# Performance work log

Hardware: AMD Instinct MI355X
Metric: run time of the kernel (lower is better)

## Reference

```python
import jax, jax.numpy as jnp
import numpy as np

INPUT_SIZE = 256
HIDDEN_SIZE = 256
B, T = 64, 4096


def setup_inputs() -> dict:
    key = jax.random.key(0)
    k_x, k_ih, k_hh, k_b = jax.random.split(key, 4)
    lim = 1.0 / np.sqrt(HIDDEN_SIZE)  # eqx LSTMCell init range
    xs = jax.random.normal(k_x, (B, T, INPUT_SIZE), dtype=jnp.float32)
    W_ih = jax.random.uniform(k_ih, (4 * HIDDEN_SIZE, INPUT_SIZE), minval=-lim, maxval=lim, dtype=jnp.float32)
    W_hh = jax.random.uniform(k_hh, (4 * HIDDEN_SIZE, HIDDEN_SIZE), minval=-lim, maxval=lim, dtype=jnp.float32)
    b = jax.random.uniform(k_b, (4 * HIDDEN_SIZE,), minval=-lim, maxval=lim, dtype=jnp.float32)
    return {"xs": xs, "W_ih": W_ih, "W_hh": W_hh, "b": b}


def reference(xs, W_ih, W_hh, b):
    # xs: [B, T, D]; eqx.nn.LSTMCell math, scanned over time, vectorized over batch.
    Bsz, Tlen, D = xs.shape
    H = W_hh.shape[1]
    # Precompute input contribution for all timesteps in one big GEMM: [T, B, 4H]
    x_gates = jnp.swapaxes(xs @ W_ih.T + b, 0, 1)

    def step(state, xg):
        h, c = state  # each [B, H]
        gates = xg + h @ W_hh.T  # [B, 4H]
        i, f, g, o = jnp.split(gates, 4, axis=-1)
        c = jax.nn.sigmoid(f) * c + jax.nn.sigmoid(i) * jnp.tanh(g)
        h = jax.nn.sigmoid(o) * jnp.tanh(c)
        return (h, c), None

    init = (jnp.zeros((Bsz, H), xs.dtype), jnp.zeros((Bsz, H), xs.dtype))
    (h, c), _ = jax.lax.scan(step, init, x_gates)
    return (h, c)
```

## Files before the change

kernel.cpp:

```cpp
#include <hip/hip_runtime.h>
#include <hip/hip_fp16.h>
#include <stdint.h>


#define LSTM_B 64
#define LSTM_T 4096
#define LSTM_D 256
#define LSTM_H 256

#define WS_HG_OFF (1u << 20)

typedef __attribute__((ext_vector_type(8))) _Float16 half8;
typedef __attribute__((ext_vector_type(4))) float f32x4;
typedef __attribute__((ext_vector_type(4))) uint32_t u32x4;

#define AST64(p, v) __hip_atomic_store((p), (v), __ATOMIC_RELAXED, __HIP_MEMORY_SCOPE_AGENT)
#define BARLG()     asm volatile("s_waitcnt lgkmcnt(0)\n\ts_barrier" ::: "memory")

static __device__ __forceinline__ float sigmoidf_(float x) {
    return 1.0f / (1.0f + __expf(-x));
}
static __device__ __forceinline__ float tanhf_(float x) {
    float ax = fabsf(x);
    float e  = __expf(-2.0f * ax);
    float t  = (1.0f - e) / (1.0f + e);
    return copysignf(t, x);
}

static __device__ __forceinline__ void ld64B_agent(const uint64_t* p, uint64_t* v) {
    u32x4 a, b, c, d;
    asm volatile(
        "global_load_dwordx4 %0, %4, off sc1\n\t"
        "global_load_dwordx4 %1, %4, off offset:16 sc1\n\t"
        "global_load_dwordx4 %2, %4, off offset:32 sc1\n\t"
        "global_load_dwordx4 %3, %4, off offset:48 sc1\n\t"
        "s_waitcnt vmcnt(0)"
        : "=&v"(a), "=&v"(b), "=&v"(c), "=&v"(d)
        : "v"(p) : "memory");
    v[0] = ((uint64_t)a.y << 32) | a.x;
    v[1] = ((uint64_t)a.w << 32) | a.z;
    v[2] = ((uint64_t)b.y << 32) | b.x;
    v[3] = ((uint64_t)b.w << 32) | b.z;
    v[4] = ((uint64_t)c.y << 32) | c.x;
    v[5] = ((uint64_t)c.w << 32) | c.z;
    v[6] = ((uint64_t)d.y << 32) | d.x;
    v[7] = ((uint64_t)d.w << 32) | d.z;
}

__global__ __launch_bounds__(256) void prep_frags(
    const float* __restrict__ W_ih, const float* __restrict__ W_hh,
    uint8_t* __restrict__ ws)
{
    int idx = blockIdx.x * blockDim.x + threadIdx.x;
    uint4* Wp = (uint4*)ws;
    int lane = idx & 63;
    int kk   = (idx >> 6) & 15;
    int T    = idx >> 10;
    int n  = T * 16 + (lane & 15);
    int r  = ((n & 3) << 8) + (n >> 2);
    int kb = 32 * kk + 4 * (lane >> 4);
    uint32_t u[4];
    #pragma unroll
    for (int h = 0; h < 4; ++h) {
        uint32_t lohi[2];
        #pragma unroll
        for (int e = 0; e < 2; ++e) {
            int j = 2 * h + e;
            int k = kb + (j & 3) + 16 * (j >> 2);
            float v = (k < 256) ? W_hh[r * 256 + k] : W_ih[r * 256 + (k - 256)];
            lohi[e] = (uint32_t)__half_as_ushort(__float2half(v));
        }
        u[h] = lohi[0] | (lohi[1] << 16);
    }
    Wp[idx] = make_uint4(u[0], u[1], u[2], u[3]);
    if (idx < 32768) ((uint32_t*)(ws + WS_HG_OFF))[idx] = 0u;
}

__global__ __launch_bounds__(256, 1) void lstm_r15(
    const float* __restrict__ xs,
    const float* __restrict__ bias_g,
    uint8_t* __restrict__ ws,
    float* __restrict__ out)
{
    const int tid = threadIdx.x;
    const int l   = tid & 63;
    const int w   = tid >> 6;
    const int g   = blockIdx.x & 7;
    const int p   = blockIdx.x >> 3;

    const uint4* WF = (const uint4*)ws;
    uint64_t* hg64  = (uint64_t*)(ws + WS_HG_OFF);

    __shared__ uint4 hx[16 * 64];

    uint4 wf[4][16];
    #pragma unroll
    for (int tl = 0; tl < 4; ++tl) {
        int T = p * 16 + w * 4 + tl;
        #pragma unroll
        for (int kk = 0; kk < 16; ++kk)
            wf[tl][kk] = WF[(T * 16 + kk) * 64 + l];
    }
    #pragma unroll
    for (int tl = 0; tl < 4; ++tl)
        #pragma unroll
        for (int kk = 0; kk < 16; ++kk)
            asm volatile("" : "+v"(wf[tl][kk].x), "+v"(wf[tl][kk].y),
                              "+v"(wf[tl][kk].z), "+v"(wf[tl][kk].w));

    const int  c2   = l & 3;
    const int  qa   = l >> 4;
    const bool c2b0 = (c2 & 1) != 0, c2b1 = (c2 & 2) != 0;
    const int  m_ew = 4 * qa + c2;
    float bias[4];
    int   jj[4];
    #pragma unroll
    for (int tl = 0; tl < 4; ++tl) {
        int T    = p * 16 + w * 4 + tl;
        int slot = T * 16 + (l & 15);
        int r    = ((slot & 3) << 8) + (slot >> 2);
        bias[tl] = bias_g[r];
        jj[tl]   = slot >> 2;
    }

    const int m_s = tid >> 4;
    const int d0  = (tid & 15) * 16;
    const float* xrow = xs + (size_t)(8 * g + (m_s & 7)) * LSTM_T * LSTM_D + d0;

    hx[tid]       = make_uint4(0, 0, 0, 0);
    hx[tid + 256] = make_uint4(0, 0, 0, 0);
    hx[tid + 512] = make_uint4(0, 0, 0, 0);
    hx[tid + 768] = make_uint4(0, 0, 0, 0);
    float4 xb[2][4];
    if (m_s < 8) {
        #pragma unroll
        for (int i = 0; i < 4; ++i) {
            float4 xv = ((const float4*)xrow)[i];
            __half2 h0 = __floats2half2_rn(xv.x, xv.y);
            __half2 h1 = __floats2half2_rn(xv.z, xv.w);
            uint64_t v = (uint64_t)__builtin_bit_cast(uint32_t, h0)
                       | ((uint64_t)__builtin_bit_cast(uint32_t, h1) << 32);
            int k0 = 256 + d0 + 4 * i;
            int kk = k0 >> 5, off = k0 & 31;
            int q = (off & 15) >> 2, hi = off >> 4;
            int slot = (m_s + 16 * q) ^ ((2 * kk) & 63);
            *(uint64_t*)((uint8_t*)hx + kk * 1024 + slot * 16 + hi * 8) = v;
        }
        #pragma unroll
        for (int i = 0; i < 4; ++i) xb[0][i] = ((const float4*)(xrow + (size_t)1 * LSTM_D))[i];
        #pragma unroll
        for (int i = 0; i < 4; ++i) xb[1][i] = ((const float4*)(xrow + (size_t)2 * LSTM_D))[i];
    }
    BARLG();

    f32x4 accA[4], accB[4];
    {
        uint4 afx[8];
        #pragma unroll
        for (int kx = 0; kx < 8; ++kx) {
            int kk = kx + 8;
            afx[kx] = hx[kk * 64 + (l ^ ((2 * kk) & 63))];
        }
        #pragma unroll
        for (int tl = 0; tl < 4; ++tl)
            accA[tl] = (f32x4){bias[tl], bias[tl], bias[tl], bias[tl]};
        #pragma unroll
        for (int kx = 0; kx < 8; ++kx) {
            half8 a = __builtin_bit_cast(half8, afx[kx]);
            #pragma unroll
            for (int tl = 0; tl < 4; ++tl)
                accA[tl] = __builtin_amdgcn_mfma_f32_16x16x32_f16(
                    a, __builtin_bit_cast(half8, wf[tl][kx + 8]), accA[tl], 0, 0, 0);
        }
    }

    float cst[4] = {0, 0, 0, 0}, hst[4] = {0, 0, 0, 0};

#define STEP(T_, PAR, ACC_C, ACC_N) do {                                            \
                    \
    uint4 afh[8];                                                                   \
    _Pragma("unroll")                                                               \
    for (int kk = 0; kk < 8; ++kk)                                                  \
        afh[kk] = hx[kk * 64 + (l ^ ((2 * kk) & 63))];                              \
    _Pragma("unroll")                                                               \
    for (int kk = 0; kk < 8; ++kk) {                                                \
        half8 a = __builtin_bit_cast(half8, afh[kk]);                               \
        _Pragma("unroll")                                                           \
        for (int tl = 0; tl < 4; ++tl)                                              \
            ACC_C[tl] = __builtin_amdgcn_mfma_f32_16x16x32_f16(                     \
                a, __builtin_bit_cast(half8, wf[tl][kk]), ACC_C[tl], 0, 0, 0);      \
    }                                                                               \
    uint32_t hpair[4];                                                              \
    _Pragma("unroll")                                                               \
    for (int tl = 0; tl < 4; ++tl) {                                                \
        f32x4 a = ACC_C[tl];                                                        \
        float s01  = c2b0 ? a.y : a.x;                                              \
        float s23  = c2b0 ? a.w : a.z;                                              \
        float s01b = c2b0 ? a.x : a.y;                                              \
        float s23b = c2b0 ? a.z : a.w;                                              \
        float own = c2b1 ? s23  : s01;                                              \
        float v1  = c2b1 ? s23b : s01b;                                             \
        float v2  = c2b1 ? s01  : s23;                                              \
        float v3  = c2b1 ? s01b : s23b;                                             \
        float r1 = __shfl_xor(v1, 1, 64);                                           \
        float r2 = __shfl_xor(v2, 2, 64);                                           \
        float r3 = __shfl_xor(v3, 3, 64);                                           \
        float gi = c2b1 ? (c2b0 ? r3 : r2) : (c2b0 ? r1 : own);                     \
        float gf = c2b1 ? (c2b0 ? r2 : r3) : (c2b0 ? own : r1);                     \
        float gg = c2b1 ? (c2b0 ? r1 : own) : (c2b0 ? r3 : r2);                     \
        float go = c2b1 ? (c2b0 ? own : r1) : (c2b0 ? r2 : r3);                     \
        float cc = cst[tl];                                                         \
        cc = sigmoidf_(gf) * cc + sigmoidf_(gi) * tanhf_(gg);                       \
        float hh = sigmoidf_(go) * tanhf_(cc);                                      \
        cst[tl] = cc; hst[tl] = hh;                                                 \
        uint32_t u  = (uint32_t)__half_as_ushort(__float2half(hh));                 \
        uint32_t up = (uint32_t)__shfl_xor((int)u, 4, 64);                          \
        hpair[tl] = (u & 0xffffu) | (up << 16);                                     \
    }                                                                               \
    {                                                                               \
        const int buf = (PAR) ^ 1;                                                  \
        if (l < 32 && (l & 4) == 0) {                                               \
            uint64_t* hgrow = hg64 + (((size_t)g * 2 + buf) * 8 + m_ew) * 128;      \
            const uint64_t tagw = ((uint64_t)(uint32_t)(T_ + 1)) << 32;             \
            _Pragma("unroll")                                                       \
            for (int tl = 0; tl < 4; ++tl)                                          \
                AST64(&hgrow[jj[tl] >> 1], tagw | (uint64_t)hpair[tl]);             \
        }                                                                           \
                            \
        if (m_s < 8) {                                                              \
            _Pragma("unroll")                                                       \
            for (int i = 0; i < 4; ++i) {                                           \
                float4 xv = xb[PAR][i];                                             \
                __half2 h0 = __floats2half2_rn(xv.x, xv.y);                         \
                __half2 h1 = __floats2half2_rn(xv.z, xv.w);                         \
                uint64_t v = (uint64_t)__builtin_bit_cast(uint32_t, h0)             \
                           | ((uint64_t)__builtin_bit_cast(uint32_t, h1) << 32);    \
                int k0 = 256 + d0 + 4 * i;                                          \
                int kk = k0 >> 5, off = k0 & 31;                                    \
                int q = (off & 15) >> 2, hi = off >> 4;                             \
                int slot = (m_s + 16 * q) ^ ((2 * kk) & 63);                        \
                *(uint64_t*)((uint8_t*)hx + kk * 1024 + slot * 16 + hi * 8) = v;    \
            }                                                                       \
            int tn = (T_ + 3 < LSTM_T) ? T_ + 3 : T_;                               \
            const float4* nx = (const float4*)(xrow + (size_t)tn * LSTM_D);         \
            _Pragma("unroll")                                                       \
            for (int i = 0; i < 4; ++i) xb[PAR][i] = nx[i];                         \
        }                                                                           \
        BARLG();          \
                                      \
        uint4 afx[8];                                                               \
        _Pragma("unroll")                                                           \
        for (int kx = 0; kx < 8; ++kx) {                                            \
            int kk = kx + 8;                                                        \
            afx[kx] = hx[kk * 64 + (l ^ ((2 * kk) & 63))];                          \
        }                                                                           \
           \
        if (m_s < 8) {                                                              \
            const uint32_t tgt = (uint32_t)(T_ + 1);                                \
            uint64_t* hgr = hg64 + (((size_t)g * 2 + buf) * 8 + m_s) * 128          \
                          + (d0 >> 1);                                              \
            uint64_t hv[8];                                                         \
            ld64B_agent(hgr, hv);                                                   \
            int spin = 0;                                                           \
            while (true) {                                                          \
                bool ok = true;                                                     \
                _Pragma("unroll")                                                   \
                for (int i = 0; i < 8; ++i) ok &= ((uint32_t)(hv[i] >> 32) >= tgt); \
                if (ok || ++spin > 2000) break;                                     \
                ld64B_agent(hgr, hv);                                               \
            }                                                                       \
            _Pragma("unroll")                                                       \
            for (int i = 0; i < 8; ++i) {                                           \
                uint32_t pr = (uint32_t)hv[i];                                      \
                int k0 = d0 + 2 * i;                                                \
                int kk = k0 >> 5, off = k0 & 31;                                    \
                int q = (off & 15) >> 2, hi = off >> 4;                             \
                int slot = (m_s + 16 * q) ^ ((2 * kk) & 63);                        \
                *(uint32_t*)((uint8_t*)hx + kk * 1024 + slot * 16 + hi * 8          \
                             + ((off & 3) << 1)) = pr;                              \
            }                                                                       \
        }                                                                           \
                    \
        _Pragma("unroll")                                                           \
        for (int tl = 0; tl < 4; ++tl)                                              \
            ACC_N[tl] = (f32x4){bias[tl], bias[tl], bias[tl], bias[tl]};            \
        _Pragma("unroll")                                                           \
        for (int kx = 0; kx < 8; ++kx) {                                            \
            half8 a = __builtin_bit_cast(half8, afx[kx]);                           \
            _Pragma("unroll")                                                       \
            for (int tl = 0; tl < 4; ++tl)                                          \
                ACC_N[tl] = __builtin_amdgcn_mfma_f32_16x16x32_f16(                 \
                    a, __builtin_bit_cast(half8, wf[tl][kx + 8]), ACC_N[tl],        \
                    0, 0, 0);                                                       \
        }                                                                           \
        BARLG();              \
    }                                                                               \
} while (0)

    for (int t = 0; t < LSTM_T; t += 2) {
        STEP(t,     0, accA, accB);
        STEP(t + 1, 1, accB, accA);
    }
#undef STEP

    if (m_ew < 8) {
        #pragma unroll
        for (int tl = 0; tl < 4; ++tl) {
            int gb = 8 * g + m_ew;
            out[gb * LSTM_H + jj[tl]]                   = hst[tl];
            out[LSTM_B * LSTM_H + gb * LSTM_H + jj[tl]] = cst[tl];
        }
    }
}

extern "C" void kernel_launch(void* const* d_in, const int* in_sizes, int n_in,
                              void* d_out, int out_size, void* d_ws, size_t ws_size,
                              hipStream_t stream) {
    const float* xs   = (const float*)d_in[0];
    const float* W_ih = (const float*)d_in[1];
    const float* W_hh = (const float*)d_in[2];
    const float* b    = (const float*)d_in[3];
    float* out = (float*)d_out;
    uint8_t* ws = (uint8_t*)d_ws;

    prep_frags<<<256, 256, 0, stream>>>(W_ih, W_hh, ws);
    lstm_r15<<<32, 256, 0, stream>>>(xs, b, ws, out);
}
```

Before: 11.80 ms.

## Split LSTM into chunked input-GEMM prepass and per-block batch recurrence

Replaces the single 32-block recurrence kernel, which exchanged h between blocks through tagged global-memory spinning, with two phases per time chunk. An xg_prep kernel precomputes the input gate contributions (x·W_ih + b) as fp16 into workspace. An lstm_rec kernel then runs 4 blocks of 512 threads, each owning 16 batch rows end to end, so h exchange happens in shared memory with block barriers instead of cross-block global synchronisation. W_hh fragments are split across registers, LDS, and per-step global reloads. The trade-offs are that each timestep now runs on far fewer CUs, x-gates are stored in fp16, and the path depends on workspace size, falling back to the old kernel when too little is available.

```diff
diff --git a/kernel.cpp b/kernel.cpp
--- a/kernel.cpp
+++ b/kernel.cpp
@@ -8,13 +8,17 @@
 #define LSTM_D 256
 #define LSTM_H 256
 
-#define WS_HG_OFF (1u << 20)
+#define WS_HG_OFF 0x100000u
+#define WS_HST    0x120000u
+#define WS_CST    0x128000u
+#define WS_XG     0x200000u
 
 typedef __attribute__((ext_vector_type(8))) _Float16 half8;
 typedef __attribute__((ext_vector_type(4))) float f32x4;
 typedef __attribute__((ext_vector_type(4))) uint32_t u32x4;
 
 #define AST64(p, v) __hip_atomic_store((p), (v), __ATOMIC_RELAXED, __HIP_MEMORY_SCOPE_AGENT)
+#define ALD64(p)    __hip_atomic_load((p), __ATOMIC_RELAXED, __HIP_MEMORY_SCOPE_AGENT)
 #define BARLG()     asm volatile("s_waitcnt lgkmcnt(0)\n\ts_barrier" ::: "memory")
 
 static __device__ __forceinline__ float sigmoidf_(float x) {
@@ -25,26 +29,6 @@
     float e  = __expf(-2.0f * ax);
     float t  = (1.0f - e) / (1.0f + e);
     return copysignf(t, x);
-}
-
-static __device__ __forceinline__ void ld64B_agent(const uint64_t* p, uint64_t* v) {
-    u32x4 a, b, c, d;
-    asm volatile(
-        "global_load_dwordx4 %0, %4, off sc1\n\t"
-        "global_load_dwordx4 %1, %4, off offset:16 sc1\n\t"
-        "global_load_dwordx4 %2, %4, off offset:32 sc1\n\t"
-        "global_load_dwordx4 %3, %4, off offset:48 sc1\n\t"
-        "s_waitcnt vmcnt(0)"
-        : "=&v"(a), "=&v"(b), "=&v"(c), "=&v"(d)
-        : "v"(p) : "memory");
-    v[0] = ((uint64_t)a.y << 32) | a.x;
-    v[1] = ((uint64_t)a.w << 32) | a.z;
-    v[2] = ((uint64_t)b.y << 32) | b.x;
-    v[3] = ((uint64_t)b.w << 32) | b.z;
-    v[4] = ((uint64_t)c.y << 32) | c.x;
-    v[5] = ((uint64_t)c.w << 32) | c.z;
-    v[6] = ((uint64_t)d.y << 32) | d.x;
-    v[7] = ((uint64_t)d.w << 32) | d.z;
 }
 
 __global__ __launch_bounds__(256) void prep_frags(
@@ -74,13 +58,327 @@
     }
     Wp[idx] = make_uint4(u[0], u[1], u[2], u[3]);
     if (idx < 32768) ((uint32_t*)(ws + WS_HG_OFF))[idx] = 0u;
+    if (idx < 24576) ((uint32_t*)(ws + WS_HST))[idx]   = 0u;
+}
+
+__global__ __launch_bounds__(256, 1) void xg_prep(
+    const float* __restrict__ xs, const float* __restrict__ bias_g,
+    uint8_t* __restrict__ ws, int tbase, int CH)
+{
+    const int tid = threadIdx.x;
+    const int l   = tid & 63;
+    const int wv  = tid >> 6;
+    const int gg  = blockIdx.x >> 3;
+    const int cs  = blockIdx.x & 7;
+    const int T0  = cs * 8 + wv * 2;
+
+    const uint4* WF = (const uint4*)ws;
+    uint2* xg = (uint2*)(ws + WS_XG) + (size_t)gg * CH * 64 * 64;
+
+    __shared__ __align__(16) uint8_t hxp[8 * 64 * 16];
+
+    uint4 wfx[2][8];
+    #pragma unroll
+    for (int t2 = 0; t2 < 2; ++t2)
+        #pragma unroll
+        for (int kk = 0; kk < 8; ++kk)
+            wfx[t2][kk] = WF[((T0 + t2) * 16 + 8 + kk) * 64 + l];
+    #pragma unroll
+    for (int t2 = 0; t2 < 2; ++t2)
+        #pragma unroll
+        for (int kk = 0; kk < 8; ++kk)
+            asm volatile("" : "+v"(wfx[t2][kk].x), "+v"(wfx[t2][kk].y),
+                              "+v"(wfx[t2][kk].z), "+v"(wfx[t2][kk].w));
+
+    float biasv[2];
+    #pragma unroll
+    for (int t2 = 0; t2 < 2; ++t2) {
+        int slot = (T0 + t2) * 16 + (l & 15);
+        biasv[t2] = bias_g[((slot & 3) << 8) + (slot >> 2)];
+    }
+
+    const int m_s = tid >> 4;
+    const int d0  = (tid & 15) * 16;
+    const float* xrow = xs + (size_t)(16 * gg + m_s) * LSTM_T * LSTM_D + d0;
+
+    float4 xb[4];
+    #pragma unroll
+    for (int i = 0; i < 4; ++i)
+        xb[i] = ((const float4*)(xrow + (size_t)tbase * LSTM_D))[i];
+
+    for (int tloc = 0; tloc < CH; ++tloc) {
+        #pragma unroll
+        for (int i = 0; i < 4; ++i) {
+            float4 xv = xb[i];
+            __half2 h0 = __floats2half2_rn(xv.x, xv.y);
+            __half2 h1 = __floats2half2_rn(xv.z, xv.w);
+            uint64_t v = (uint64_t)__builtin_bit_cast(uint32_t, h0)
+                       | ((uint64_t)__builtin_bit_cast(uint32_t, h1) << 32);
+            int k0 = d0 + 4 * i;
+            int kk = k0 >> 5, off = k0 & 31;
+            int q = (off & 15) >> 2, hi = off >> 4;
+            int slot = (m_s + 16 * q) ^ ((2 * kk) & 63);
+            *(uint64_t*)(hxp + kk * 1024 + slot * 16 + hi * 8) = v;
+        }
+        {
+            int tn = tbase + tloc + 1; if (tn > LSTM_T - 1) tn = LSTM_T - 1;
+            const float4* nx = (const float4*)(xrow + (size_t)tn * LSTM_D);
+            #pragma unroll
+            for (int i = 0; i < 4; ++i) xb[i] = nx[i];
+        }
+        BARLG();
+
+        uint4 af[8];
+        #pragma unroll
+        for (int kk = 0; kk < 8; ++kk)
+            af[kk] = *(const uint4*)(hxp + (kk * 64 + (l ^ ((2 * kk) & 63))) * 16);
+
+        f32x4 acc[2];
+        #pragma unroll
+        for (int t2 = 0; t2 < 2; ++t2)
+            acc[t2] = (f32x4){biasv[t2], biasv[t2], biasv[t2], biasv[t2]};
+        #pragma unroll
+        for (int kk = 0; kk < 8; ++kk) {
+            half8 a = __builtin_bit_cast(half8, af[kk]);
+            #pragma unroll
+            for (int t2 = 0; t2 < 2; ++t2)
+                acc[t2] = __builtin_amdgcn_mfma_f32_16x16x32_f16(
+                    a, __builtin_bit_cast(half8, wfx[t2][kk]), acc[t2], 0, 0, 0);
+        }
+        #pragma unroll
+        for (int t2 = 0; t2 < 2; ++t2) {
+            __half2 lo = __floats2half2_rn(acc[t2].x, acc[t2].y);
+            __half2 hi = __floats2half2_rn(acc[t2].z, acc[t2].w);
+            xg[(((size_t)tloc) * 64 + T0 + t2) * 64 + l] =
+                make_uint2(__builtin_bit_cast(uint32_t, lo),
+                           __builtin_bit_cast(uint32_t, hi));
+        }
+        BARLG();
+    }
+}
+
+__global__ __launch_bounds__(512, 2) void lstm_rec(
+    uint8_t* __restrict__ ws, float* __restrict__ out, int CH, int final_ch)
+{
+    const int tid = threadIdx.x;
+    const int l   = tid & 63;
+    const int wv  = tid >> 6;
+    const int gg  = blockIdx.x;
+
+    const uint4* WF = (const uint4*)ws;
+    uint32_t* hstate = (uint32_t*)(ws + WS_HST) + (size_t)gg * 16 * 128;
+    float*    cstate = (float*)(ws + WS_CST)    + (size_t)gg * 16 * 256;
+    const uint2* xg  = (const uint2*)(ws + WS_XG) + (size_t)gg * CH * 64 * 64;
+
+    __shared__ uint4 wl[2 * 64 * 64];
+    __shared__ __align__(16) uint8_t hA[8 * 64 * 16];
+
+    #pragma unroll
+    for (int j2 = 0; j2 < 16; ++j2) {
+        int idx = j2 * 512 + tid;
+        int kkL = idx >> 12, T = (idx >> 6) & 63, ll = idx & 63;
+        wl[idx] = WF[(T * 16 + 3 + kkL) * 64 + ll];
+    }
+
+    uint4 wfh[8][3];
+    #pragma unroll
+    for (int tl = 0; tl < 8; ++tl) {
+        int T = wv * 8 + tl;
+        #pragma unroll
+        for (int kk = 0; kk < 3; ++kk)
+            wfh[tl][kk] = WF[(T * 16 + kk) * 64 + l];
+    }
+    #pragma unroll
+    for (int tl = 0; tl < 8; ++tl)
+        #pragma unroll
+        for (int kk = 0; kk < 3; ++kk)
+            asm volatile("" : "+v"(wfh[tl][kk].x), "+v"(wfh[tl][kk].y),
+                              "+v"(wfh[tl][kk].z), "+v"(wfh[tl][kk].w));
+
+    const int  c2   = l & 3;
+    const int  qa   = l >> 4;
+    const bool c2b0 = (c2 & 1) != 0, c2b1 = (c2 & 2) != 0;
+    const int  m_ew = 4 * qa + c2;
+    int jj[8];
+    #pragma unroll
+    for (int tl = 0; tl < 8; ++tl) {
+        int slot = (wv * 8 + tl) * 16 + (l & 15);
+        jj[tl] = slot >> 2;
+    }
+
+    if (tid < 256) {
+        int m_s = tid >> 4, d0 = (tid & 15) * 16;
+        const uint32_t* hr = hstate + m_s * 128 + (d0 >> 1);
+        #pragma unroll
+        for (int i = 0; i < 8; ++i) {
+            uint32_t pr = hr[i];
+            int k0 = d0 + 2 * i;
+            int kk = k0 >> 5, off = k0 & 31;
+            int q = (off & 15) >> 2, hi = off >> 4;
+            int slot = (m_s + 16 * q) ^ ((2 * kk) & 63);
+            *(uint32_t*)(hA + kk * 1024 + slot * 16 + hi * 8 + ((off & 3) << 1)) = pr;
+        }
+    }
+    float c[8];
+    #pragma unroll
+    for (int tl = 0; tl < 8; ++tl) c[tl] = cstate[m_ew * 256 + jj[tl]];
+
+    BARLG();
+
+    uint2 xgv[8];
+    #pragma unroll
+    for (int tl = 0; tl < 8; ++tl)
+        xgv[tl] = xg[((size_t)0 * 64 + wv * 8 + tl) * 64 + l];
+
+    uint32_t hpair[8];
+
+    for (int tloc = 0; tloc < CH; ++tloc) {
+        uint4 af[8];
+        #pragma unroll
+        for (int kk = 0; kk < 8; ++kk)
+            af[kk] = *(const uint4*)(hA + (kk * 64 + (l ^ ((2 * kk) & 63))) * 16);
+
+        const bool fin = final_ch && (tloc == CH - 1);
+
+        #pragma unroll
+        for (int hp = 0; hp < 2; ++hp) {
+            const int base = hp * 4;
+            uint4 s5[4], s6[4];
+            #pragma unroll
+            for (int i = 0; i < 4; ++i) {
+                int T = wv * 8 + base + i;
+                s5[i] = WF[(T * 16 + 5) * 64 + l];
+                s6[i] = WF[(T * 16 + 6) * 64 + l];
+            }
+            f32x4 acc[4];
+            #pragma unroll
+            for (int i = 0; i < 4; ++i) {
+                uint2 v = xgv[base + i];
+                float2 f0 = __half22float2(__builtin_bit_cast(__half2, v.x));
+                float2 f1 = __half22float2(__builtin_bit_cast(__half2, v.y));
+                acc[i] = (f32x4){f0.x, f0.y, f1.x, f1.y};
+            }
+            #pragma unroll
+            for (int kk = 0; kk < 3; ++kk) {
+                half8 a = __builtin_bit_cast(half8, af[kk]);
+                #pragma unroll
+                for (int i = 0; i < 4; ++i)
+                    acc[i] = __builtin_amdgcn_mfma_f32_16x16x32_f16(
+                        a, __builtin_bit_cast(half8, wfh[base + i][kk]), acc[i], 0, 0, 0);
+            }
+            uint4 s7[4];
+            #pragma unroll
+            for (int i = 0; i < 4; ++i)
+                s7[i] = WF[((wv * 8 + base + i) * 16 + 7) * 64 + l];
+            #pragma unroll
+            for (int kkL = 0; kkL < 2; ++kkL) {
+                half8 a = __builtin_bit_cast(half8, af[3 + kkL]);
+                #pragma unroll
+                for (int i = 0; i < 4; ++i) {
+                    uint4 wb = wl[(kkL * 64 + wv * 8 + base + i) * 64 + l];
+                    acc[i] = __builtin_amdgcn_mfma_f32_16x16x32_f16(
+                        a, __builtin_bit_cast(half8, wb), acc[i], 0, 0, 0);
+                }
+            }
+            {
+                half8 a5 = __builtin_bit_cast(half8, af[5]);
+                half8 a6 = __builtin_bit_cast(half8, af[6]);
+                half8 a7 = __builtin_bit_cast(half8, af[7]);
+                #pragma unroll
+                for (int i = 0; i < 4; ++i)
+                    acc[i] = __builtin_amdgcn_mfma_f32_16x16x32_f16(
+                        a5, __builtin_bit_cast(half8, s5[i]), acc[i], 0, 0, 0);
+                #pragma unroll
+                for (int i = 0; i < 4; ++i)
+                    acc[i] = __builtin_amdgcn_mfma_f32_16x16x32_f16(
+                        a6, __builtin_bit_cast(half8, s6[i]), acc[i], 0, 0, 0);
+                #pragma unroll
+                for (int i = 0; i < 4; ++i)
+                    acc[i] = __builtin_amdgcn_mfma_f32_16x16x32_f16(
+                        a7, __builtin_bit_cast(half8, s7[i]), acc[i], 0, 0, 0);
+            }
+            #pragma unroll
+            for (int i = 0; i < 4; ++i) {
+                int tl = base + i;
+                f32x4 a = acc[i];
+                float s01  = c2b0 ? a.y : a.x;
+                float s23  = c2b0 ? a.w : a.z;
+                float s01b = c2b0 ? a.x : a.y;
+                float s23b = c2b0 ? a.z : a.w;
+                float own = c2b1 ? s23  : s01;
+                float v1  = c2b1 ? s23b : s01b;
+                float v2  = c2b1 ? s01  : s23;
+                float v3  = c2b1 ? s01b : s23b;
+                float r1 = __shfl_xor(v1, 1, 64);
+                float r2 = __shfl_xor(v2, 2, 64);
+                float r3 = __shfl_xor(v3, 3, 64);
+                float gi = c2b1 ? (c2b0 ? r3 : r2) : (c2b0 ? r1 : own);
+                float gf = c2b1 ? (c2b0 ? r2 : r3) : (c2b0 ? own : r1);
+                float gg2 = c2b1 ? (c2b0 ? r1 : own) : (c2b0 ? r3 : r2);
+                float go = c2b1 ? (c2b0 ? own : r1) : (c2b0 ? r2 : r3);
+                float cc = c[tl];
+                cc = sigmoidf_(gf) * cc + sigmoidf_(gi) * tanhf_(gg2);
+                float hh = sigmoidf_(go) * tanhf_(cc);
+                c[tl] = cc;
+                uint32_t u  = (uint32_t)__half_as_ushort(__float2half(hh));
+                uint32_t up = (uint32_t)__shfl_xor((int)u, 4, 64);
+                hpair[tl] = (u & 0xffffu) | (up << 16);
+                if (fin) {
+                    int b = 16 * gg + m_ew;
+                    out[b * LSTM_H + jj[tl]]                        = hh;
+                    out[LSTM_B * LSTM_H + b * LSTM_H + jj[tl]]      = cc;
+                }
+            }
+        }
+
+        if (tloc + 1 < CH) {
+            #pragma unroll
+            for (int tl = 0; tl < 8; ++tl)
+                xgv[tl] = xg[((size_t)(tloc + 1) * 64 + wv * 8 + tl) * 64 + l];
+        }
+
+        BARLG();
+        if ((l & 4) == 0) {
+            #pragma unroll
+            for (int tl = 0; tl < 8; ++tl) {
+                int k0 = jj[tl];
+                int kk = k0 >> 5, off = k0 & 31;
+                int q = (off & 15) >> 2, hi = off >> 4;
+                int slot = (m_ew + 16 * q) ^ ((2 * kk) & 63);
+                *(uint32_t*)(hA + kk * 1024 + slot * 16 + hi * 8 + ((off & 3) << 1)) = hpair[tl];
+            }
+        }
+        BARLG();
+    }
+
+    if ((l & 4) == 0) {
+        #pragma unroll
+        for (int tl = 0; tl < 8; ++tl)
+            hstate[m_ew * 128 + (jj[tl] >> 1)] = hpair[tl];
+    }
+    #pragma unroll
+    for (int tl = 0; tl < 8; ++tl) cstate[m_ew * 256 + jj[tl]] = c[tl];
+}
+
+static __device__ __forceinline__ void ld64B_agent(const uint64_t* p, uint64_t* v) {
+    u32x4 a, b, cq, d;
+    asm volatile(
+        "global_load_dwordx4 %0, %4, off sc1\n\t"
+        "global_load_dwordx4 %1, %4, off offset:16 sc1\n\t"
+        "global_load_dwordx4 %2, %4, off offset:32 sc1\n\t"
+        "global_load_dwordx4 %3, %4, off offset:48 sc1\n\t"
+        "s_waitcnt vmcnt(0)"
+        : "=&v"(a), "=&v"(b), "=&v"(cq), "=&v"(d)
+        : "v"(p) : "memory");
+    v[0] = ((uint64_t)a.y << 32) | a.x;   v[1] = ((uint64_t)a.w << 32) | a.z;
+    v[2] = ((uint64_t)b.y << 32) | b.x;   v[3] = ((uint64_t)b.w << 32) | b.z;
+    v[4] = ((uint64_t)cq.y << 32) | cq.x; v[5] = ((uint64_t)cq.w << 32) | cq.z;
+    v[6] = ((uint64_t)d.y << 32) | d.x;   v[7] = ((uint64_t)d.w << 32) | d.z;
 }
 
 __global__ __launch_bounds__(256, 1) void lstm_r15(
-    const float* __restrict__ xs,
-    const float* __restrict__ bias_g,
-    uint8_t* __restrict__ ws,
-    float* __restrict__ out)
+    const float* __restrict__ xs, const float* __restrict__ bias_g,
+    uint8_t* __restrict__ ws, float* __restrict__ out)
 {
     const int tid = threadIdx.x;
     const int l   = tid & 63;
@@ -177,7 +475,6 @@
     float cst[4] = {0, 0, 0, 0}, hst[4] = {0, 0, 0, 0};
 
 #define STEP(T_, PAR, ACC_C, ACC_N) do {                                            \
-                    \
     uint4 afh[8];                                                                   \
     _Pragma("unroll")                                                               \
     for (int kk = 0; kk < 8; ++kk)                                                  \
@@ -226,7 +523,6 @@
             for (int tl = 0; tl < 4; ++tl)                                          \
                 AST64(&hgrow[jj[tl] >> 1], tagw | (uint64_t)hpair[tl]);             \
         }                                                                           \
-                            \
         if (m_s < 8) {                                                              \
             _Pragma("unroll")                                                       \
             for (int i = 0; i < 4; ++i) {                                           \
@@ -246,15 +542,13 @@
             _Pragma("unroll")                                                       \
             for (int i = 0; i < 4; ++i) xb[PAR][i] = nx[i];                         \
         }                                                                           \
-        BARLG();          \
-                                      \
+        BARLG();                                                                    \
         uint4 afx[8];                                                               \
         _Pragma("unroll")                                                           \
         for (int kx = 0; kx < 8; ++kx) {                                            \
             int kk = kx + 8;                                                        \
             afx[kx] = hx[kk * 64 + (l ^ ((2 * kk) & 63))];                          \
         }                                                                           \
-           \
         if (m_s < 8) {                                                              \
             const uint32_t tgt = (uint32_t)(T_ + 1);                                \
             uint64_t* hgr = hg64 + (((size_t)g * 2 + buf) * 8 + m_s) * 128          \
@@ -280,7 +574,6 @@
                              + ((off & 3) << 1)) = pr;                              \
             }                                                                       \
         }                                                                           \
-                    \
         _Pragma("unroll")                                                           \
         for (int tl = 0; tl < 4; ++tl)                                              \
             ACC_N[tl] = (f32x4){bias[tl], bias[tl], bias[tl], bias[tl]};            \
@@ -293,7 +586,7 @@
                     a, __builtin_bit_cast(half8, wf[tl][kx + 8]), ACC_N[tl],        \
                     0, 0, 0);                                                       \
         }                                                                           \
-        BARLG();              \
+        BARLG();                                                                    \
     }                                                                               \
 } while (0)
 
@@ -324,5 +617,19 @@
     uint8_t* ws = (uint8_t*)d_ws;
 
     prep_frags<<<256, 256, 0, stream>>>(W_ih, W_hh, ws);
-    lstm_r15<<<32, 256, 0, stream>>>(xs, b, ws, out);
-}
+
+    const size_t per_t = 131072;
+    int CH = 0;
+    if      (ws_size >= (size_t)WS_XG + 4096 * per_t) CH = 4096;
+    else if (ws_size >= (size_t)WS_XG + 1024 * per_t) CH = 1024;
+    else if (ws_size >= (size_t)WS_XG +  256 * per_t) CH = 256;
+
+    if (CH) {
+        for (int tb = 0; tb < LSTM_T; tb += CH) {
+            xg_prep<<<32, 256, 0, stream>>>(xs, b, ws, tb, CH);
+            lstm_rec<<<4, 512, 0, stream>>>(ws, out, CH, (tb + CH == LSTM_T) ? 1 : 0);
+        }
+    } else {
+        lstm_r15<<<32, 256, 0, stream>>>(xs, b, ws, out);
+    }
+}
```

Result: slower. 31.63 ms (+168.1%).
